# Performance work log

Hardware: AMD Instinct MI355X
Metric: run time of the kernel (lower is better)

Reference implementation:

```python
import jax, jax.numpy as jnp
import numpy as np

N = 100_000      # nodes
E = 1_600_000    # directed edges (before self-loops)
F_IN = 256       # input node features
H = 128          # hidden_dim
HEADS = 2
C_HEAD = H // HEADS  # 64, GATConv out_channels per head
G = 128          # graphs in batch
NCLS = 10
NEG_SLOPE = 0.2  # PyG GATConv default


def setup_inputs() -> dict:
    key = jax.random.key(0)
    ks = jax.random.split(key, 20)
    p = lambda k, shape: (jax.random.normal(k, shape, jnp.float32) * 0.05)
    x = jax.random.normal(ks[0], (N, F_IN), jnp.float32)
    edge_index = jax.random.randint(ks[1], (2, E), 0, N, dtype=jnp.int64)
    batch = jnp.sort(jax.random.randint(ks[2], (N,), 0, G, dtype=jnp.int64))
    return dict(
        x=x, edge_index=edge_index, batch=batch,
        pre_w=p(ks[3], (F_IN, H)), pre_b=p(ks[4], (H,)),
        w1=p(ks[5], (H, H)), asrc1=p(ks[6], (HEADS, C_HEAD)), adst1=p(ks[7], (HEADS, C_HEAD)), b1=p(ks[8], (H,)),
        w2=p(ks[9], (H, H)), asrc2=p(ks[10], (HEADS, C_HEAD)), adst2=p(ks[11], (HEADS, C_HEAD)), b2=p(ks[12], (H,)),
        post_w1=p(ks[13], (H, H)), post_b1=p(ks[14], (H,)),
        post_w2=p(ks[15], (H, NCLS)), post_b2=p(ks[16], (NCLS,)),
    )


def _gat_conv(h_in, w, a_src, a_dst, b, src, dst):
    # h: [N, heads, c]
    h = (h_in @ w).reshape(N, HEADS, C_HEAD)
    alpha_src = jnp.sum(h * a_src, axis=-1)  # [N, heads]
    alpha_dst = jnp.sum(h * a_dst, axis=-1)  # [N, heads]
    e = jax.nn.leaky_relu(alpha_src[src] + alpha_dst[dst], NEG_SLOPE)  # [E+N, heads]
    # numerically stable softmax over incoming edges of each destination node
    m = jax.ops.segment_max(e, dst, num_segments=N)
    ex = jnp.exp(e - m[dst])
    denom = jax.ops.segment_sum(ex, dst, num_segments=N)
    alpha = ex / denom[dst]                                           # [E+N, heads]
    out = jax.ops.segment_sum(h[src] * alpha[:, :, None], dst, num_segments=N)
    return out.reshape(N, H) + b  # concat heads + bias


def reference(x, edge_index, batch, pre_w, pre_b,
              w1, asrc1, adst1, b1, w2, asrc2, adst2, b2,
              post_w1, post_b1, post_w2, post_b2):
    # PyG GATConv default add_self_loops=True
    loop = jnp.arange(N, dtype=edge_index.dtype)
    src = jnp.concatenate([edge_index[0], loop])
    dst = jnp.concatenate([edge_index[1], loop])

    h = jax.nn.relu(x @ pre_w + pre_b)
    reprs = jax.ops.segment_sum(h, batch, num_segments=G)
    h = jax.nn.relu(_gat_conv(h, w1, asrc1, adst1, b1, src, dst))
    reprs = reprs + jax.ops.segment_sum(h, batch, num_segments=G)
    h = jax.nn.relu(_gat_conv(h, w2, asrc2, adst2, b2, src, dst))
    reprs = reprs + jax.ops.segment_sum(h, batch, num_segments=G)
    z = jax.nn.relu(reprs @ post_w1 + post_b1) @ post_w2 + post_b2
    return jax.nn.log_softmax(z, axis=-1)
```

## Files before the change

### kernel.cpp

```cpp
#include <hip/hip_runtime.h>
#include <hip/hip_bf16.h>
#include <math.h>

#define NNODES 100000
#define NEDGES 1600000
#define FIN 256
#define HDIM 128
#define NGRAPH 128
#define NCLS 10
#define NEG 0.2f

#define NBUCK 98
#define EPB 4096
#define EBLK ((NEDGES + EPB - 1) / EPB)

typedef short bf8 __attribute__((ext_vector_type(8)));
typedef float f4 __attribute__((ext_vector_type(4)));
typedef float f2v __attribute__((ext_vector_type(2)));

__device__ __forceinline__ float lrelu(float x) { return x > 0.f ? x : NEG * x; }

__device__ __forceinline__ unsigned short f2bf(float f) {
  union { float f; unsigned int u; } v; v.f = f;
  unsigned int r = v.u + 0x7fffu + ((v.u >> 16) & 1u);
  return (unsigned short)(r >> 16);
}
__device__ __forceinline__ float bf2f(unsigned short u) {
  union { unsigned int u; float f; } v; v.u = ((unsigned int)u) << 16; return v.f;
}
__device__ __forceinline__ float fast_rcp(float x) {
  float r;
  asm("v_rcp_f32 %0, %1" : "=v"(r) : "v"(x));
  return r;
}
__device__ __forceinline__ unsigned cvt_pk_bf16(float lo, float hi) {
  unsigned r;
  asm("v_cvt_pk_bf16_f32 %0, %1, %2" : "=v"(r) : "v"(lo), "v"(hi));
  return r;
}
__device__ __forceinline__ unsigned short pk_fp8(float a, float b) {
  return (unsigned short)__builtin_amdgcn_cvt_pk_fp8_f32(a, b, 0, false);
}
__device__ __forceinline__ f2v pk_unpack_fp8(unsigned p) {
#if __has_builtin(__builtin_amdgcn_cvt_pk_f32_fp8)
  return __builtin_amdgcn_cvt_pk_f32_fp8((int)p, false);
#else
  f2v r;
  r.x = __builtin_amdgcn_cvt_f32_fp8(p, 0);
  r.y = __builtin_amdgcn_cvt_f32_fp8(p, 1);
  return r;
#endif
}

__global__ __launch_bounds__(256) void convert_transpose(const float* __restrict__ w,
                                                         unsigned short* __restrict__ wt,
                                                         int K) {
  int i = blockIdx.x * 256 + threadIdx.x;
  if (i >= K * 128) return;
  int k = i >> 7, n = i & 127;
  wt[n * K + k] = f2bf(w[(size_t)k * 128 + n]);
}

template<int K, int ABF16>
__global__ __launch_bounds__(256) void gemm_bres(const void* __restrict__ Av,
                                                 const unsigned short* __restrict__ Bt,
                                                 const float* __restrict__ bias,
                                                 unsigned short* __restrict__ Cb,
                                                 unsigned short* __restrict__ Cp,
                                                 const float* __restrict__ a_src,
                                                 const float* __restrict__ a_dst,
                                                 float* __restrict__ o_as,
                                                 float* __restrict__ o_ad,
                                                 int M, int dorelu) {
  __shared__ bf8 Bs[2048];
  constexpr int NCH = K / 128;
  int tid = threadIdx.x;
  int wv = tid >> 6, lane = tid & 63;
  int quad = lane >> 4, m16 = lane & 15;
  int row0 = blockIdx.x * 128;

  int rA0 = row0 + wv * 16 + m16; if (rA0 > M - 1) rA0 = M - 1;
  int rA1 = rA0 + 64; if (rA1 > M - 1) rA1 = M - 1;
  int cOff = quad * 8;

  auto cvt8 = [&](float4 a, float4 b) -> bf8 {
    union { bf8 v; unsigned u[4]; } r;
    r.u[0] = cvt_pk_bf16(a.x, a.y); r.u[1] = cvt_pk_bf16(a.z, a.w);
    r.u[2] = cvt_pk_bf16(b.x, b.y); r.u[3] = cvt_pk_bf16(b.z, b.w);
    return r.v;
  };

  f4 acc[16];
#pragma unroll
  for (int b = 0; b < 16; ++b) acc[b] = (f4){0.f, 0.f, 0.f, 0.f};

  for (int ch = 0; ch < NCH; ++ch) {
    if (ch) __syncthreads();
#pragma unroll
    for (int jj = 0; jj < 8; ++jj) {
      int j = jj * 256 + tid;
      int n = ((j >> 6) & 7) * 16 + (j & 15);
      int k = ch * 128 + (j >> 9) * 32 + ((j >> 4) & 3) * 8;
      Bs[j] = *reinterpret_cast<const bf8*>(&Bt[(size_t)n * K + k]);
    }
    __syncthreads();
#pragma unroll
    for (int kt = 0; kt < 4; ++kt) {
      int kb = ch * 128 + kt * 32;
      bf8 a0, a1;
      if (ABF16) {
        a0 = *reinterpret_cast<const bf8*>((const unsigned short*)Av + (size_t)rA0 * K + kb + cOff);
        a1 = *reinterpret_cast<const bf8*>((const unsigned short*)Av + (size_t)rA1 * K + kb + cOff);
      } else {
        const float* p0 = (const float*)Av + (size_t)rA0 * K + kb + cOff;
        const float* p1 = (const float*)Av + (size_t)rA1 * K + kb + cOff;
        float4 x0 = *reinterpret_cast<const float4*>(p0);
        float4 x1 = *reinterpret_cast<const float4*>(p0 + 4);
        float4 y0 = *reinterpret_cast<const float4*>(p1);
        float4 y1 = *reinterpret_cast<const float4*>(p1 + 4);
        a0 = cvt8(x0, x1);
        a1 = cvt8(y0, y1);
      }
#pragma unroll
      for (int tn = 0; tn < 8; ++tn) {
        bf8 bfm = Bs[kt * 512 + tn * 64 + lane];
        acc[tn]     = __builtin_amdgcn_mfma_f32_16x16x32_bf16(a0, bfm, acc[tn], 0, 0, 0);
        acc[8 + tn] = __builtin_amdgcn_mfma_f32_16x16x32_bf16(a1, bfm, acc[8 + tn], 0, 0, 0);
      }
    }
  }

  if (Cp) {
    if (a_src) {
      float aS[8], aD[8];
#pragma unroll
      for (int tn = 0; tn < 4; ++tn) {
        aS[tn]     = a_src[tn * 16 + m16];
        aS[tn + 4] = a_src[64 + tn * 16 + m16];
        aD[tn]     = a_dst[tn * 16 + m16];
        aD[tn + 4] = a_dst[64 + tn * 16 + m16];
      }
#pragma unroll
      for (int mt = 0; mt < 2; ++mt) {
#pragma unroll
        for (int r = 0; r < 4; ++r) {
          int row = row0 + mt * 64 + wv * 16 + quad * 4 + r;
          float ps0 = 0.f, ps1 = 0.f, pd0 = 0.f, pd1 = 0.f;
#pragma unroll
          for (int tn = 0; tn < 4; ++tn) {
            float v0 = acc[mt * 8 + tn][r], v1 = acc[mt * 8 + tn + 4][r];
            ps0 = fmaf(v0, aS[tn], ps0);
            ps1 = fmaf(v1, aS[tn + 4], ps1);
            pd0 = fmaf(v0, aD[tn], pd0);
            pd1 = fmaf(v1, aD[tn + 4], pd1);
          }
#pragma unroll
          for (int o = 8; o; o >>= 1) {
            ps0 += __shfl_xor(ps0, o); ps1 += __shfl_xor(ps1, o);
            pd0 += __shfl_xor(pd0, o); pd1 += __shfl_xor(pd1, o);
          }
          if (m16 == 0 && row < M) {
            o_as[2 * row] = ps0; o_as[2 * row + 1] = ps1;
            o_ad[2 * row] = pd0; o_ad[2 * row + 1] = pd1;
          }
        }
      }
    }
#pragma unroll
    for (int mt = 0; mt < 2; ++mt)
#pragma unroll
      for (int tn = 0; tn < 4; ++tn)
#pragma unroll
        for (int r = 0; r < 4; ++r) {
          int row = row0 + mt * 64 + wv * 16 + quad * 4 + r;
          if (row < M) {
            Cp[(size_t)row * 64 + tn * 16 + m16] =
                pk_fp8(acc[mt * 8 + tn][r], acc[mt * 8 + tn + 4][r]);
          }
        }
  } else {
#pragma unroll
    for (int mt = 0; mt < 2; ++mt)
#pragma unroll
      for (int tn = 0; tn < 8; ++tn) {
        float bv = bias ? bias[tn * 16 + m16] : 0.f;
#pragma unroll
        for (int r = 0; r < 4; ++r) {
          int row = row0 + mt * 64 + wv * 16 + quad * 4 + r;
          if (row < M) {
            float v = acc[mt * 8 + tn][r] + bv;
            if (dorelu) v = fmaxf(v, 0.f);
            Cb[(size_t)row * 128 + tn * 16 + m16] = f2bf(v);
          }
        }
      }
  }
}

__global__ void find_starts(const int* __restrict__ batch, int* __restrict__ gstart) {
  int g = threadIdx.x;
  if (g > NGRAPH) return;
  if (g == NGRAPH) { gstart[g] = NNODES; return; }
  int lo = 0, hi = NNODES;
  while (lo < hi) { int mid = (lo + hi) >> 1; if (batch[mid] < g) lo = mid + 1; else hi = mid; }
  gstart[g] = lo;
}

__global__ __launch_bounds__(256) void bin_count(const int* __restrict__ edst,
                                                 int* __restrict__ blockHist) {
  __shared__ int hist[NBUCK];
  int t = threadIdx.x, blk = blockIdx.x;
  if (t < NBUCK) hist[t] = 0;
  __syncthreads();
  int e0 = blk * EPB;
#pragma unroll
  for (int it = 0; it < EPB / 256; ++it) {
    int e = e0 + it * 256 + t;
    if (e < NEDGES) atomicAdd(&hist[((unsigned)edst[e]) >> 10], 1);
  }
  __syncthreads();
  if (t < NBUCK) blockHist[blk * NBUCK + t] = hist[t];
}

__global__ __launch_bounds__(512) void colscan(const int* __restrict__ blockHist,
                                               int* __restrict__ blockBaseCol,
                                               int* __restrict__ bucket_total) {
  __shared__ int s[512];
  int b = blockIdx.x, t = threadIdx.x;
  int v = (t < EBLK) ? blockHist[t * NBUCK + b] : 0;
  s[t] = v;
  __syncthreads();
  for (int off = 1; off < 512; off <<= 1) {
    int u = (t >= off) ? s[t - off] : 0;
    __syncthreads();
    s[t] += u;
    __syncthreads();
  }
  if (t < EBLK) blockBaseCol[b * EBLK + t] = s[t] - v;
  if (t == 511) bucket_total[b] = s[511];
}

__global__ __launch_bounds__(128) void bscan(const int* __restrict__ bucket_total,
                                             int* __restrict__ bucket_ptr) {
  __shared__ int s[128];
  int t = threadIdx.x;
  int v = (t < NBUCK) ? bucket_total[t] : 0;
  s[t] = v;
  __syncthreads();
  for (int off = 1; off < 128; off <<= 1) {
    int u = (t >= off) ? s[t - off] : 0;
    __syncthreads();
    s[t] += u;
    __syncthreads();
  }
  if (t < NBUCK) bucket_ptr[t] = s[t] - v;
  if (t == 127) bucket_ptr[NBUCK] = s[127];
}

__global__ __launch_bounds__(512) void bin_place(const int* __restrict__ esrc,
                                                 const int* __restrict__ edst,
                                                 const int* __restrict__ blockBaseCol,
                                                 const int* __restrict__ bucket_ptr,
                                                 unsigned* __restrict__ stagingG) {
  __shared__ int hist[NBUCK + 1], lbase[NBUCK + 1], lcur[NBUCK + 1], cbase[NBUCK];
  __shared__ int tmp[128];
  __shared__ uint2 st[EPB];
  int t = threadIdx.x, blk = blockIdx.x;
  if (t < NBUCK + 1) hist[t] = 0;
  __syncthreads();
  int e0 = blk * EPB;
#pragma unroll
  for (int it = 0; it < EPB / 512; ++it) {
    int e = e0 + it * 512 + t;
    int b = NBUCK;
    if (e < NEDGES) b = ((unsigned)edst[e]) >> 10;
    atomicAdd(&hist[b], 1);
  }
  __syncthreads();
  if (t < 128) tmp[t] = (t < NBUCK + 1) ? hist[t] : 0;
  __syncthreads();
  for (int off = 1; off < 128; off <<= 1) {
    int u = 0;
    if (t < 128 && t >= off) u = tmp[t - off];
    __syncthreads();
    if (t < 128) tmp[t] += u;
    __syncthreads();
  }
  if (t < NBUCK + 1) { int ex = tmp[t] - hist[t]; lbase[t] = ex; lcur[t] = ex; }
  if (t < NBUCK) cbase[t] = bucket_ptr[t] + blockBaseCol[t * EBLK + blk];
  __syncthreads();
#pragma unroll
  for (int it = 0; it < EPB / 512; ++it) {
    int e = e0 + it * 512 + t;
    unsigned s = 0, d = 0xFFFFFFFFu;
    if (e < NEDGES) { s = (unsigned)esrc[e]; d = (unsigned)edst[e]; }
    int b = (d == 0xFFFFFFFFu) ? NBUCK : (int)(d >> 10);
    int slot = atomicAdd(&lcur[b], 1);
    st[slot] = make_uint2(s, d);
  }
  __syncthreads();
  for (int i = t; i < EPB; i += 512) {
    uint2 ed = st[i];
    if (ed.y == 0xFFFFFFFFu) continue;
    int b = (int)(ed.y >> 10);
    stagingG[cbase[b] + (i - lbase[b])] = ((ed.y & 1023u) << 17) | ed.x;
  }
}

__global__ __launch_bounds__(1024) void bucket_csr_fused(const unsigned* __restrict__ stagingG,
                                                         const int* __restrict__ bucket_ptr,
                                                         int* __restrict__ row_ptr,
                                                         int* __restrict__ colv) {
  __shared__ int dl[1024];
  __shared__ int cur[1024];
  int b = blockIdx.x, t = threadIdx.x;
  dl[t] = 0;
  __syncthreads();
  int s0 = bucket_ptr[b], s1 = bucket_ptr[b + 1];
  for (int j = s0 + t; j < s1; j += 1024)
    atomicAdd(&dl[stagingG[j] >> 17], 1);
  __syncthreads();
  int myDeg = dl[t];
  for (int off = 1; off < 1024; off <<= 1) {
    int u = (t >= off) ? dl[t - off] : 0;
    __syncthreads();
    dl[t] += u;
    __syncthreads();
  }
  int rp = s0 + dl[t] - myDeg;
  cur[t] = rp;
  int n = (b << 10) + t;
  if (n < NNODES) row_ptr[n] = rp;
  if (n == NNODES - 1) row_ptr[NNODES] = rp + myDeg;
  __syncthreads();
  for (int j = s0 + t; j < s1; j += 1024) {
    unsigned v = stagingG[j];
    int pos = atomicAdd(&cur[v >> 17], 1);
    colv[pos] = (int)(v & 0x1FFFFu);
  }
}

__global__ __launch_bounds__(256) void aggregate(const unsigned short* __restrict__ hwb,
                                                 const float* __restrict__ a_s,
                                                 const float* __restrict__ a_d,
                                                 const int* __restrict__ row_ptr,
                                                 const int* __restrict__ colv,
                                                 const float* __restrict__ bias,
                                                 unsigned short* __restrict__ out) {
  __shared__ float2 wsh[256];
  int i = (blockIdx.x * 256 + threadIdx.x) >> 6;
  int lane = threadIdx.x & 63;
  if (i >= NNODES) return;
  i = __builtin_amdgcn_readfirstlane(i);
  int wbase = (threadIdx.x >> 6) * 64;

  float ad0 = a_d[2 * i], ad1 = a_d[2 * i + 1];
  int start = row_ptr[i], end = row_ptr[i + 1];
  int deg = end - start;
  float ws0 = __expf(lrelu(a_s[2 * i] + ad0));
  float ws1 = __expf(lrelu(a_s[2 * i + 1] + ad1));

  int sl = 0; float w0l = 0.f, w1l = 0.f;
  if (lane < deg) {
    sl = colv[start + lane];
    float2 av = *reinterpret_cast<const float2*>(&a_s[2 * sl]);
    w0l = __expf(lrelu(av.x + ad0));
    w1l = __expf(lrelu(av.y + ad1));
  }
  wsh[wbase + lane] = make_float2(w0l, w1l);
  float d0 = w0l, d1 = w1l;
  for (int o = 32; o; o >>= 1) { d0 += __shfl_xor(d0, o); d1 += __shfl_xor(d1, o); }
  float den0 = d0 + ws0, den1 = d1 + ws1;

  unsigned ps = hwb[(size_t)i * 64 + lane];
  f2v pv = pk_unpack_fp8(ps);
  float acc0 = ws0 * pv.x, acc1 = ws1 * pv.y;

  int dmin = deg < 64 ? deg : 64;
  int t = 0;
#define GSTEP(T)                                                               \
  {                                                                            \
    int s = __builtin_amdgcn_readlane(sl, (T));                                \
    unsigned q = hwb[(size_t)s * 64 + lane];                                   \
    float2 w = wsh[wbase + (T)];                    \
    f2v xv = pk_unpack_fp8(q);                                                 \
    acc0 = fmaf(w.x, xv.x, acc0);                                              \
    acc1 = fmaf(w.y, xv.y, acc1);                                              \
  }
  for (; t + 8 <= dmin; t += 8) {
    GSTEP(t);     GSTEP(t + 1); GSTEP(t + 2); GSTEP(t + 3);
    GSTEP(t + 4); GSTEP(t + 5); GSTEP(t + 6); GSTEP(t + 7);
  }
  for (; t < dmin; ++t) { GSTEP(t); }
#undef GSTEP

  for (int j = start + 64; j < end; ++j) {
    int s = colv[j];
    float2 av = *reinterpret_cast<const float2*>(&a_s[2 * s]);
    float w0 = __expf(lrelu(av.x + ad0));
    float w1 = __expf(lrelu(av.y + ad1));
    den0 += w0; den1 += w1;
    unsigned q = hwb[(size_t)s * 64 + lane];
    f2v xv = pk_unpack_fp8(q);
    acc0 = fmaf(w0, xv.x, acc0);
    acc1 = fmaf(w1, xv.y, acc1);
  }

  float r0 = fast_rcp(den0), r1 = fast_rcp(den1);
  float o0 = fmaxf(acc0 * r0 + bias[lane], 0.f);
  float o1 = fmaxf(acc1 * r1 + bias[64 + lane], 0.f);
  unsigned pk = cvt_pk_bf16(o0, o1);
  out[(size_t)i * 128 + lane]      = (unsigned short)pk;
  out[(size_t)i * 128 + 64 + lane] = (unsigned short)(pk >> 16);
}

#define SEG_CHUNK 128
__global__ __launch_bounds__(128) void seg_sum_fast(const unsigned short* __restrict__ h,
                                                    const int* __restrict__ batch,
                                                    const int* __restrict__ gstart,
                                                    float* __restrict__ reprs) {
  int n0 = blockIdx.x * SEG_CHUNK;
  if (n0 >= NNODES) return;
  int nend = n0 + SEG_CHUNK; if (nend > NNODES) nend = NNODES;
  int tid = threadIdx.x;
  int r = n0;
  while (r < nend) {
    int g = batch[r];
    int segend = gstart[g + 1]; if (segend > nend) segend = nend;
    float a0 = 0.f, a1 = 0.f, a2 = 0.f, a3 = 0.f;
    for (; r + 3 < segend; r += 4) {
      a0 += bf2f(h[(size_t)r * 128 + tid]);
      a1 += bf2f(h[(size_t)(r + 1) * 128 + tid]);
      a2 += bf2f(h[(size_t)(r + 2) * 128 + tid]);
      a3 += bf2f(h[(size_t)(r + 3) * 128 + tid]);
    }
    for (; r < segend; ++r) a0 += bf2f(h[(size_t)r * 128 + tid]);
    atomicAdd(&reprs[g * 128 + tid], (a0 + a1) + (a2 + a3));
  }
}

__global__ __launch_bounds__(128) void head_kernel(const float* __restrict__ reprs,
                                                   const float* __restrict__ pw1,
                                                   const float* __restrict__ pb1,
                                                   const float* __restrict__ pw2,
                                                   const float* __restrict__ pb2,
                                                   float* __restrict__ out) {
  __shared__ float r[128], t1[128], z[NCLS];
  int g = blockIdx.x, tid = threadIdx.x;
  r[tid] = reprs[g * 128 + tid];
  __syncthreads();
  float acc = pb1[tid];
  for (int k = 0; k < 128; ++k) acc = fmaf(r[k], pw1[k * 128 + tid], acc);
  t1[tid] = fmaxf(acc, 0.f);
  __syncthreads();
  if (tid < NCLS) {
    float zz = pb2[tid];
    for (int k = 0; k < 128; ++k) zz = fmaf(t1[k], pw2[k * NCLS + tid], zz);
    z[tid] = zz;
  }
  __syncthreads();
  if (tid == 0) {
    float mx = -1e30f;
    for (int c = 0; c < NCLS; ++c) mx = fmaxf(mx, z[c]);
    float s = 0.f;
    for (int c = 0; c < NCLS; ++c) s += expf(z[c] - mx);
    float ls = logf(s) + mx;
    for (int c = 0; c < NCLS; ++c) out[g * NCLS + c] = z[c] - ls;
  }
}

extern "C" void kernel_launch(void* const* d_in, const int* in_sizes, int n_in,
                              void* d_out, int out_size, void* d_ws, size_t ws_size,
                              hipStream_t stream) {
  const float* x     = (const float*)d_in[0];
  const int*   eidx  = (const int*)d_in[1];
  const int*   batch = (const int*)d_in[2];
  const float* pre_w = (const float*)d_in[3];
  const float* pre_b = (const float*)d_in[4];
  const float* w1    = (const float*)d_in[5];
  const float* asrc1 = (const float*)d_in[6];
  const float* adst1 = (const float*)d_in[7];
  const float* b1    = (const float*)d_in[8];
  const float* w2    = (const float*)d_in[9];
  const float* asrc2 = (const float*)d_in[10];
  const float* adst2 = (const float*)d_in[11];
  const float* b2    = (const float*)d_in[12];
  const float* pw1   = (const float*)d_in[13];
  const float* pb1   = (const float*)d_in[14];
  const float* pw2   = (const float*)d_in[15];
  const float* pb2   = (const float*)d_in[16];
  float* out = (float*)d_out;

  const int* esrc = eidx;
  const int* edst = eidx + NEDGES;

  char* wsp = (char*)d_ws;
  size_t off = 0;
  auto alloc = [&](size_t bytes) -> void* {
    void* p = wsp + off;
    off += (bytes + 255) & ~(size_t)255;
    return p;
  };
  unsigned short* hb  = (unsigned short*)alloc((size_t)NNODES * 128 * 2);
  unsigned short* hwb = (unsigned short*)alloc((size_t)NNODES * 64 * 2);
  float* a_s         = (float*)alloc((size_t)NNODES * 2 * 4);
  float* a_d         = (float*)alloc((size_t)NNODES * 2 * 4);
  float* reprs       = (float*)alloc((size_t)NGRAPH * 128 * 4);
  int* gstart        = (int*)alloc((NGRAPH + 1) * 4);
  int* row_ptr       = (int*)alloc(((size_t)NNODES + 1) * 4);
  int* colv          = (int*)alloc((size_t)NEDGES * 4);
  unsigned short* wt_pre = (unsigned short*)alloc((size_t)128 * FIN * 2);
  unsigned short* wt1    = (unsigned short*)alloc((size_t)128 * HDIM * 2);
  unsigned short* wt2    = (unsigned short*)alloc((size_t)128 * HDIM * 2);
  int* blockHist     = (int*)alloc((size_t)EBLK * NBUCK * 4);
  int* blockBaseCol  = (int*)alloc((size_t)NBUCK * EBLK * 4);
  int* bucket_total  = (int*)alloc(NBUCK * 4);
  int* bucket_ptr    = (int*)alloc((NBUCK + 1) * 4);
  unsigned* stagingG = (unsigned*)alloc((size_t)NEDGES * 4);

  int wb = NNODES / 4;
  int sb = (NNODES + SEG_CHUNK - 1) / SEG_CHUNK;
  int gb = (NNODES + 127) / 128;

  convert_transpose<<<(FIN * 128 + 255) / 256, 256, 0, stream>>>(pre_w, wt_pre, FIN);
  convert_transpose<<<(HDIM * 128 + 255) / 256, 256, 0, stream>>>(w1, wt1, HDIM);
  convert_transpose<<<(HDIM * 128 + 255) / 256, 256, 0, stream>>>(w2, wt2, HDIM);

  hipMemsetAsync(reprs, 0, (size_t)NGRAPH * 128 * 4, stream);
  find_starts<<<1, 256, 0, stream>>>(batch, gstart);

  bin_count<<<EBLK, 256, 0, stream>>>(edst, blockHist);
  colscan<<<NBUCK, 512, 0, stream>>>(blockHist, blockBaseCol, bucket_total);
  bscan<<<1, 128, 0, stream>>>(bucket_total, bucket_ptr);
  bin_place<<<EBLK, 512, 0, stream>>>(esrc, edst, blockBaseCol, bucket_ptr, stagingG);
  bucket_csr_fused<<<NBUCK, 1024, 0, stream>>>(stagingG, bucket_ptr, row_ptr, colv);

  gemm_bres<FIN, 0><<<gb, 256, 0, stream>>>(x, wt_pre, pre_b, hb, nullptr,
                                            nullptr, nullptr, nullptr, nullptr, NNODES, 1);
  seg_sum_fast<<<sb, 128, 0, stream>>>(hb, batch, gstart, reprs);

  gemm_bres<HDIM, 1><<<gb, 256, 0, stream>>>(hb, wt1, nullptr, nullptr, hwb,
                                             asrc1, adst1, a_s, a_d, NNODES, 0);
  aggregate<<<wb, 256, 0, stream>>>(hwb, a_s, a_d, row_ptr, colv, b1, hb);
  seg_sum_fast<<<sb, 128, 0, stream>>>(hb, batch, gstart, reprs);

  gemm_bres<HDIM, 1><<<gb, 256, 0, stream>>>(hb, wt2, nullptr, nullptr, hwb,
                                             asrc2, adst2, a_s, a_d, NNODES, 0);
  aggregate<<<wb, 256, 0, stream>>>(hwb, a_s, a_d, row_ptr, colv, b2, hb);
  seg_sum_fast<<<sb, 128, 0, stream>>>(hb, batch, gstart, reprs);

  head_kernel<<<NGRAPH, 128, 0, stream>>>(reprs, pw1, pb1, pw2, pb2, out);
}
```

Measured before the change: 479.6 us.

## Stage A tiles in swizzled LDS with coalesced loads, halve GEMM block rows

The GEMM kernel now loads the whole 64-row A tile into LDS with coalesced, row-contiguous global reads (converting fp32 to bf16 on the fly), using an XOR swizzle to avoid bank conflicts. It no longer has each lane read strided 16-byte fragments directly from global memory. Block height drops from 128 to 64 rows, doubling the grid and halving the accumulators per thread. The aim is better global coalescing and occupancy. In exchange, B is reloaded twice as often in total, and LDS use grows (32KB for K=256).

```diff
diff --git a/kernel.cpp b/kernel.cpp
--- a/kernel.cpp
+++ b/kernel.cpp
@@ -62,70 +62,86 @@
 }
 
 template<int K, int ABF16>
-__global__ __launch_bounds__(256) void gemm_bres(const void* __restrict__ Av,
-                                                 const unsigned short* __restrict__ Bt,
-                                                 const float* __restrict__ bias,
-                                                 unsigned short* __restrict__ Cb,
-                                                 unsigned short* __restrict__ Cp,
-                                                 const float* __restrict__ a_src,
-                                                 const float* __restrict__ a_dst,
-                                                 float* __restrict__ o_as,
-                                                 float* __restrict__ o_ad,
-                                                 int M, int dorelu) {
-  __shared__ bf8 Bs[2048];
-  constexpr int NCH = K / 128;
+__global__ __launch_bounds__(256) void gemm_cstage(const void* __restrict__ Av,
+                                                   const unsigned short* __restrict__ Bt,
+                                                   const float* __restrict__ bias,
+                                                   unsigned short* __restrict__ Cb,
+                                                   unsigned short* __restrict__ Cp,
+                                                   const float* __restrict__ a_src,
+                                                   const float* __restrict__ a_dst,
+                                                   float* __restrict__ o_as,
+                                                   float* __restrict__ o_ad,
+                                                   int M, int dorelu) {
+  constexpr int NKT = K / 32;
+  __shared__ alignas(16) char AL[NKT * 256 * 16];
+  __shared__ alignas(16) char BL[4 * 512 * 16];
   int tid = threadIdx.x;
   int wv = tid >> 6, lane = tid & 63;
   int quad = lane >> 4, m16 = lane & 15;
-  int row0 = blockIdx.x * 128;
-
-  int rA0 = row0 + wv * 16 + m16; if (rA0 > M - 1) rA0 = M - 1;
-  int rA1 = rA0 + 64; if (rA1 > M - 1) rA1 = M - 1;
-  int cOff = quad * 8;
-
-  auto cvt8 = [&](float4 a, float4 b) -> bf8 {
-    union { bf8 v; unsigned u[4]; } r;
-    r.u[0] = cvt_pk_bf16(a.x, a.y); r.u[1] = cvt_pk_bf16(a.z, a.w);
-    r.u[2] = cvt_pk_bf16(b.x, b.y); r.u[3] = cvt_pk_bf16(b.z, b.w);
-    return r.v;
+  int row0 = blockIdx.x * 64;
+
+  if (ABF16) {
+    const unsigned short* A = (const unsigned short*)Av;
+    constexpr int UPR = K / 8;
+#pragma unroll
+    for (int i = 0; i < (64 * UPR) / 256; ++i) {
+      int m = i * 256 + tid;
+      int row = m / UPR;
+      int u = m & (UPR - 1);
+      int rr = row0 + row; if (rr > M - 1) rr = M - 1;
+      bf8 v = *(const bf8*)&A[(size_t)rr * K + u * 8];
+      int kt = u >> 2, q = u & 3;
+      int dst = (((kt * 256) + (row >> 4) * 64 + q * 16 + (row & 15)) * 16) ^ ((kt & 7) << 4);
+      *(bf8*)(AL + dst) = v;
+    }
+  } else {
+    const float* A = (const float*)Av;
+    constexpr int UPRF = K / 4;
+#pragma unroll
+    for (int i = 0; i < (64 * UPRF) / 256; ++i) {
+      int m = i * 256 + tid;
+      int row = m / UPRF;
+      int u = m & (UPRF - 1);
+      int rr = row0 + row; if (rr > M - 1) rr = M - 1;
+      float4 v = *(const float4*)&A[(size_t)rr * K + u * 4];
+      int kt = u >> 3, q = (u >> 1) & 3;
+      int dst = ((kt * 256 + (row >> 4) * 64 + q * 16 + (row & 15)) * 16 + (u & 1) * 8) ^ ((kt & 7) << 4);
+      uint2 w; w.x = cvt_pk_bf16(v.x, v.y); w.y = cvt_pk_bf16(v.z, v.w);
+      *(uint2*)(AL + dst) = w;
+    }
+  }
+
+  auto stageB = [&](int ch) {
+#pragma unroll
+    for (int i = 0; i < 8; ++i) {
+      int m = i * 256 + tid;
+      int nrow = m >> 4;
+      int u = m & 15;
+      bf8 v = *(const bf8*)&Bt[(size_t)nrow * K + ch * 128 + u * 8];
+      int ktl = u >> 2;
+      int dst = ((ktl * 512 + (nrow >> 4) * 64 + (u & 3) * 16 + (nrow & 15)) * 16) ^ (ktl << 4);
+      *(bf8*)(BL + dst) = v;
+    }
   };
 
-  f4 acc[16];
-#pragma unroll
-  for (int b = 0; b < 16; ++b) acc[b] = (f4){0.f, 0.f, 0.f, 0.f};
-
+  f4 acc[8];
+#pragma unroll
+  for (int b = 0; b < 8; ++b) acc[b] = (f4){0.f, 0.f, 0.f, 0.f};
+
+  stageB(0);
+  __syncthreads();
+  constexpr int NCH = K / 128;
+#pragma unroll
   for (int ch = 0; ch < NCH; ++ch) {
-    if (ch) __syncthreads();
-#pragma unroll
-    for (int jj = 0; jj < 8; ++jj) {
-      int j = jj * 256 + tid;
-      int n = ((j >> 6) & 7) * 16 + (j & 15);
-      int k = ch * 128 + (j >> 9) * 32 + ((j >> 4) & 3) * 8;
-      Bs[j] = *reinterpret_cast<const bf8*>(&Bt[(size_t)n * K + k]);
-    }
-    __syncthreads();
-#pragma unroll
-    for (int kt = 0; kt < 4; ++kt) {
-      int kb = ch * 128 + kt * 32;
-      bf8 a0, a1;
-      if (ABF16) {
-        a0 = *reinterpret_cast<const bf8*>((const unsigned short*)Av + (size_t)rA0 * K + kb + cOff);
-        a1 = *reinterpret_cast<const bf8*>((const unsigned short*)Av + (size_t)rA1 * K + kb + cOff);
-      } else {
-        const float* p0 = (const float*)Av + (size_t)rA0 * K + kb + cOff;
-        const float* p1 = (const float*)Av + (size_t)rA1 * K + kb + cOff;
-        float4 x0 = *reinterpret_cast<const float4*>(p0);
-        float4 x1 = *reinterpret_cast<const float4*>(p0 + 4);
-        float4 y0 = *reinterpret_cast<const float4*>(p1);
-        float4 y1 = *reinterpret_cast<const float4*>(p1 + 4);
-        a0 = cvt8(x0, x1);
-        a1 = cvt8(y0, y1);
-      }
+    if (ch) { __syncthreads(); stageB(ch); __syncthreads(); }
+#pragma unroll
+    for (int ktl = 0; ktl < 4; ++ktl) {
+      int kt = ch * 4 + ktl;
+      bf8 af = *(const bf8*)(AL + ((((kt * 256) + wv * 64 + lane) * 16) ^ ((kt & 7) << 4)));
 #pragma unroll
       for (int tn = 0; tn < 8; ++tn) {
-        bf8 bfm = Bs[kt * 512 + tn * 64 + lane];
-        acc[tn]     = __builtin_amdgcn_mfma_f32_16x16x32_bf16(a0, bfm, acc[tn], 0, 0, 0);
-        acc[8 + tn] = __builtin_amdgcn_mfma_f32_16x16x32_bf16(a1, bfm, acc[8 + tn], 0, 0, 0);
+        bf8 bm = *(const bf8*)(BL + (((ktl * 512 + tn * 64 + lane) * 16) ^ (ktl << 4)));
+        acc[tn] = __builtin_amdgcn_mfma_f32_16x16x32_bf16(af, bm, acc[tn], 0, 0, 0);
       }
     }
   }
@@ -141,59 +157,51 @@
         aD[tn + 4] = a_dst[64 + tn * 16 + m16];
       }
 #pragma unroll
-      for (int mt = 0; mt < 2; ++mt) {
-#pragma unroll
-        for (int r = 0; r < 4; ++r) {
-          int row = row0 + mt * 64 + wv * 16 + quad * 4 + r;
-          float ps0 = 0.f, ps1 = 0.f, pd0 = 0.f, pd1 = 0.f;
-#pragma unroll
-          for (int tn = 0; tn < 4; ++tn) {
-            float v0 = acc[mt * 8 + tn][r], v1 = acc[mt * 8 + tn + 4][r];
-            ps0 = fmaf(v0, aS[tn], ps0);
-            ps1 = fmaf(v1, aS[tn + 4], ps1);
-            pd0 = fmaf(v0, aD[tn], pd0);
-            pd1 = fmaf(v1, aD[tn + 4], pd1);
-          }
-#pragma unroll
-          for (int o = 8; o; o >>= 1) {
-            ps0 += __shfl_xor(ps0, o); ps1 += __shfl_xor(ps1, o);
-            pd0 += __shfl_xor(pd0, o); pd1 += __shfl_xor(pd1, o);
-          }
-          if (m16 == 0 && row < M) {
-            o_as[2 * row] = ps0; o_as[2 * row + 1] = ps1;
-            o_ad[2 * row] = pd0; o_ad[2 * row + 1] = pd1;
-          }
+      for (int r = 0; r < 4; ++r) {
+        int row = row0 + wv * 16 + quad * 4 + r;
+        float ps0 = 0.f, ps1 = 0.f, pd0 = 0.f, pd1 = 0.f;
+#pragma unroll
+        for (int tn = 0; tn < 4; ++tn) {
+          float v0 = acc[tn][r], v1 = acc[tn + 4][r];
+          ps0 = fmaf(v0, aS[tn], ps0);
+          ps1 = fmaf(v1, aS[tn + 4], ps1);
+          pd0 = fmaf(v0, aD[tn], pd0);
+          pd1 = fmaf(v1, aD[tn + 4], pd1);
+        }
+#pragma unroll
+        for (int o = 8; o; o >>= 1) {
+          ps0 += __shfl_xor(ps0, o); ps1 += __shfl_xor(ps1, o);
+          pd0 += __shfl_xor(pd0, o); pd1 += __shfl_xor(pd1, o);
+        }
+        if (m16 == 0 && row < M) {
+          o_as[2 * row] = ps0; o_as[2 * row + 1] = ps1;
+          o_ad[2 * row] = pd0; o_ad[2 * row + 1] = pd1;
         }
       }
     }
 #pragma unroll
-    for (int mt = 0; mt < 2; ++mt)
-#pragma unroll
-      for (int tn = 0; tn < 4; ++tn)
-#pragma unroll
-        for (int r = 0; r < 4; ++r) {
-          int row = row0 + mt * 64 + wv * 16 + quad * 4 + r;
-          if (row < M) {
-            Cp[(size_t)row * 64 + tn * 16 + m16] =
-                pk_fp8(acc[mt * 8 + tn][r], acc[mt * 8 + tn + 4][r]);
-          }
-        }
-  } else {
-#pragma unroll
-    for (int mt = 0; mt < 2; ++mt)
-#pragma unroll
-      for (int tn = 0; tn < 8; ++tn) {
-        float bv = bias ? bias[tn * 16 + m16] : 0.f;
-#pragma unroll
-        for (int r = 0; r < 4; ++r) {
-          int row = row0 + mt * 64 + wv * 16 + quad * 4 + r;
-          if (row < M) {
-            float v = acc[mt * 8 + tn][r] + bv;
-            if (dorelu) v = fmaxf(v, 0.f);
-            Cb[(size_t)row * 128 + tn * 16 + m16] = f2bf(v);
-          }
+    for (int tn = 0; tn < 4; ++tn)
+#pragma unroll
+      for (int r = 0; r < 4; ++r) {
+        int row = row0 + wv * 16 + quad * 4 + r;
+        if (row < M) {
+          Cp[(size_t)row * 64 + tn * 16 + m16] = pk_fp8(acc[tn][r], acc[tn + 4][r]);
         }
       }
+  } else {
+#pragma unroll
+    for (int tn = 0; tn < 8; ++tn) {
+      float bv = bias ? bias[tn * 16 + m16] : 0.f;
+#pragma unroll
+      for (int r = 0; r < 4; ++r) {
+        int row = row0 + wv * 16 + quad * 4 + r;
+        if (row < M) {
+          float v = acc[tn][r] + bv;
+          if (dorelu) v = fmaxf(v, 0.f);
+          Cb[(size_t)row * 128 + tn * 16 + m16] = f2bf(v);
+        }
+      }
+    }
   }
 }
 
@@ -520,7 +528,7 @@
 
   int wb = NNODES / 4;
   int sb = (NNODES + SEG_CHUNK - 1) / SEG_CHUNK;
-  int gb = (NNODES + 127) / 128;
+  int gb = (NNODES + 63) / 64;
 
   convert_transpose<<<(FIN * 128 + 255) / 256, 256, 0, stream>>>(pre_w, wt_pre, FIN);
   convert_transpose<<<(HDIM * 128 + 255) / 256, 256, 0, stream>>>(w1, wt1, HDIM);
@@ -535,17 +543,17 @@
   bin_place<<<EBLK, 512, 0, stream>>>(esrc, edst, blockBaseCol, bucket_ptr, stagingG);
   bucket_csr_fused<<<NBUCK, 1024, 0, stream>>>(stagingG, bucket_ptr, row_ptr, colv);
 
-  gemm_bres<FIN, 0><<<gb, 256, 0, stream>>>(x, wt_pre, pre_b, hb, nullptr,
-                                            nullptr, nullptr, nullptr, nullptr, NNODES, 1);
+  gemm_cstage<FIN, 0><<<gb, 256, 0, stream>>>(x, wt_pre, pre_b, hb, nullptr,
+                                              nullptr, nullptr, nullptr, nullptr, NNODES, 1);
   seg_sum_fast<<<sb, 128, 0, stream>>>(hb, batch, gstart, reprs);
 
-  gemm_bres<HDIM, 1><<<gb, 256, 0, stream>>>(hb, wt1, nullptr, nullptr, hwb,
-                                             asrc1, adst1, a_s, a_d, NNODES, 0);
+  gemm_cstage<HDIM, 1><<<gb, 256, 0, stream>>>(hb, wt1, nullptr, nullptr, hwb,
+                                               asrc1, adst1, a_s, a_d, NNODES, 0);
   aggregate<<<wb, 256, 0, stream>>>(hwb, a_s, a_d, row_ptr, colv, b1, hb);
   seg_sum_fast<<<sb, 128, 0, stream>>>(hb, batch, gstart, reprs);
 
-  gemm_bres<HDIM, 1><<<gb, 256, 0, stream>>>(hb, wt2, nullptr, nullptr, hwb,
-                                             asrc2, adst2, a_s, a_d, NNODES, 0);
+  gemm_cstage<HDIM, 1><<<gb, 256, 0, stream>>>(hb, wt2, nullptr, nullptr, hwb,
+                                               asrc2, adst2, a_s, a_d, NNODES, 0);
   aggregate<<<wb, 256, 0, stream>>>(hwb, a_s, a_d, row_ptr, colv, b2, hb);
   seg_sum_fast<<<sb, 128, 0, stream>>>(hb, batch, gstart, reprs);
 
```

Result: no change. 470.3 us (-1.9%).
